# Performance work log

Hardware: AMD Instinct MI355X
Metric: run time of the kernel (lower is better)

## Reference

```python
import jax, jax.numpy as jnp
import numpy as np

N = 100000
E = 6400000
F_IN = 128
N_CLASSES = 16


def _glorot(key, shape):
    fan_in, fan_out = shape[0], shape[1]
    lim = (6.0 / (fan_in + fan_out)) ** 0.5
    return jax.random.uniform(key, shape, jnp.float32, -lim, lim)


def setup_inputs() -> dict:
    key = jax.random.key(0)
    ks = jax.random.split(key, 12)
    x = jax.random.normal(ks[0], (N, F_IN), jnp.float32)
    edge_index = jax.random.randint(ks[1], (2, E), 0, N, jnp.int64)
    return {
        "x": x,
        "W1": _glorot(ks[2], (F_IN, 16)), "b1": jnp.zeros((16,), jnp.float32),
        "W2": _glorot(ks[3], (16, 32)), "b2": jnp.zeros((32,), jnp.float32),
        "Wf1": _glorot(ks[4], (32, 64)), "bf1": jnp.zeros((64,), jnp.float32),
        "Wf2": _glorot(ks[5], (64, 32)), "bf2": jnp.zeros((32,), jnp.float32),
        "Wf3": _glorot(ks[6], (32, N_CLASSES)), "bf3": jnp.zeros((N_CLASSES,), jnp.float32),
        "edge_index": edge_index,
    }


def gcn_conv(x, edge_index, W, b):
    """GCNConv: D^-1/2 (A+I) D^-1/2 X W + b (self-loops added)."""
    h = x @ W  # transform first (small hidden dim), then aggregate
    loop = jnp.arange(N, dtype=edge_index.dtype)
    src = jnp.concatenate([edge_index[0], loop])
    dst = jnp.concatenate([edge_index[1], loop])
    deg = jax.ops.segment_sum(jnp.ones_like(dst, dtype=h.dtype), dst, num_segments=N)
    dinv = jnp.where(deg > 0, jax.lax.rsqrt(jnp.maximum(deg, 1.0)), 0.0)
    norm = dinv[src] * dinv[dst]  # [E+N]
    msg = h[src] * norm[:, None]  # gather + scale
    out = jax.ops.segment_sum(msg, dst, num_segments=N)  # scatter-add
    return out + b


def reference(x, W1, b1, W2, b2, Wf1, bf1, Wf2, bf2, Wf3, bf3, edge_index):
    h = jax.nn.relu(gcn_conv(x, edge_index, W1, b1))
    h = jax.nn.relu(gcn_conv(h, edge_index, W2, b2))
    h = jax.nn.relu(h @ Wf1 + bf1)
    h = jax.nn.relu(h @ Wf2 + bf2)
    return h @ Wf3 + bf3
```

## Files before the change

kernel.cpp:

```cpp
#include <hip/hip_runtime.h>
#include <hip/hip_bf16.h>
#include <math.h>

#define F_IN 128
#define H1c 16
#define H2c 32
#define H3c 64
#define H4c 32
#define NCc 16

#define BUCKET 256
#define BSH 8
#define BMASK 255u
#define BMAXB 512
#define GP 512

typedef unsigned int u32;

static __device__ __forceinline__ void ldsAddU(u32* p, u32 v) {
    __hip_atomic_fetch_add(p, v, __ATOMIC_RELAXED, __HIP_MEMORY_SCOPE_WORKGROUP);
}
static __device__ __forceinline__ u32 ldsAddURtn(u32* p, u32 v) {
    return __hip_atomic_fetch_add(p, v, __ATOMIC_RELAXED, __HIP_MEMORY_SCOPE_WORKGROUP);
}

__global__ __launch_bounds__(256) void k_detect(const u32* __restrict__ ei, u32* __restrict__ flags) {
    __shared__ int nz;
    if (threadIdx.x == 0) nz = 0;
    __syncthreads();
    for (int i = threadIdx.x; 2 * i + 1 < 8192; i += blockDim.x) {
        if (ei[2 * i + 1] != 0u) atomicAdd(&nz, 1);
    }
    __syncthreads();
    if (threadIdx.x == 0) flags[0] = (nz == 0) ? 2u : 1u;
}

__global__ __launch_bounds__(1024) void k_hist(const u32* __restrict__ ei, int E, int B,
                                               const u32* __restrict__ flags,
                                               u32* __restrict__ cntGB) {
    __shared__ u32 hist[BMAXB];
    for (int t = threadIdx.x; t < B; t += 1024) hist[t] = 0u;
    __syncthreads();
    u32 strd = flags[0];
    int chunk = (E + GP - 1) / GP;
    int e0 = blockIdx.x * chunk;
    int e1 = min(E, e0 + chunk);
    for (int e = e0 + threadIdx.x; e < e1; e += 1024) {
        u32 d = ei[((size_t)E + (size_t)e) * strd];
        ldsAddU(&hist[d >> BSH], 1u);
    }
    __syncthreads();
    for (int t = threadIdx.x; t < B; t += 1024)
        cntGB[(size_t)blockIdx.x * B + t] = hist[t];
}

__global__ __launch_bounds__(GP) void k_scanG(const u32* __restrict__ cntGB, int B,
                                              u32* __restrict__ gbOff, u32* __restrict__ total) {
    __shared__ u32 s[GP];
    int b = blockIdx.x;
    u32 v = cntGB[(size_t)threadIdx.x * B + b];
    s[threadIdx.x] = v;
    __syncthreads();
    for (int o = 1; o < GP; o <<= 1) {
        u32 t = (threadIdx.x >= (u32)o) ? s[threadIdx.x - o] : 0u;
        __syncthreads();
        s[threadIdx.x] += t;
        __syncthreads();
    }
    gbOff[(size_t)threadIdx.x * B + b] = s[threadIdx.x] - v;
    if (threadIdx.x == GP - 1) total[b] = s[GP - 1];
}

__global__ __launch_bounds__(256) void k_scanB(const u32* __restrict__ total, int B,
                                               u32* __restrict__ bstartP) {
    __shared__ u32 s[256];
    int per = (B + 255) / 256;
    int i0 = threadIdx.x * per;
    int iend = min(B, i0 + per);
    u32 sum = 0u;
    for (int i = i0; i < iend; ++i) sum += (total[i] + 3u) & ~3u;
    s[threadIdx.x] = sum;
    __syncthreads();
    for (int o = 1; o < 256; o <<= 1) {
        u32 t = (threadIdx.x >= (u32)o) ? s[threadIdx.x - o] : 0u;
        __syncthreads();
        s[threadIdx.x] += t;
        __syncthreads();
    }
    u32 run = s[threadIdx.x] - sum;
    for (int i = i0; i < iend; ++i) { bstartP[i] = run; run += (total[i] + 3u) & ~3u; }
}

__global__ __launch_bounds__(1024) void k_part(const u32* __restrict__ ei, int E, int B,
                                               const u32* __restrict__ flags,
                                               const u32* __restrict__ gbOff,
                                               const u32* __restrict__ bstartP,
                                               u32* __restrict__ bbuf) {
    __shared__ u32 cur[BMAXB];
    for (int t = threadIdx.x; t < B; t += 1024)
        cur[t] = bstartP[t] + gbOff[(size_t)blockIdx.x * B + t];
    __syncthreads();
    u32 strd = flags[0];
    int chunk = (E + GP - 1) / GP;
    int e0 = blockIdx.x * chunk;
    int e1 = min(E, e0 + chunk);
    for (int e = e0 + threadIdx.x; e < e1; e += 1024) {
        u32 sidx = ei[(size_t)e * strd];
        u32 d = ei[((size_t)E + (size_t)e) * strd];
        u32 p = atomicAdd(&cur[d >> BSH], 1u);
        bbuf[p] = (sidx << BSH) | (d & BMASK);
    }
}

__global__ __launch_bounds__(1024) void k_csr(const u32* __restrict__ bbuf,
                                              const u32* __restrict__ bstartP,
                                              const u32* __restrict__ total, int N,
                                              u32* __restrict__ cnt, u32* __restrict__ off,
                                              float* __restrict__ dinv, u32* __restrict__ perm) {
    __shared__ u32 ncnt[BUCKET];
    __shared__ u32 sc[BUCKET];
    __shared__ u32 ncur[BUCKET];
    int b = blockIdx.x;
    u32 base = bstartP[b], tot = total[b];
    if (threadIdx.x < BUCKET) ncnt[threadIdx.x] = 0u;
    __syncthreads();
    u32 nv4 = tot >> 2;
    for (u32 q = threadIdx.x; q < nv4; q += 1024) {
        uint4 e4 = *reinterpret_cast<const uint4*>(bbuf + base + q * 4);
        ldsAddU(&ncnt[e4.x & BMASK], 1u);
        ldsAddU(&ncnt[e4.y & BMASK], 1u);
        ldsAddU(&ncnt[e4.z & BMASK], 1u);
        ldsAddU(&ncnt[e4.w & BMASK], 1u);
    }
    u32 i0 = (nv4 << 2) + threadIdx.x;
    if (i0 < tot) ldsAddU(&ncnt[bbuf[base + i0] & BMASK], 1u);
    __syncthreads();
    u32 v = 0u;
    if (threadIdx.x < BUCKET) { v = ncnt[threadIdx.x]; sc[threadIdx.x] = v; }
    __syncthreads();
    for (int o = 1; o < BUCKET; o <<= 1) {
        u32 t = 0u;
        if (threadIdx.x < BUCKET && threadIdx.x >= (u32)o) t = sc[threadIdx.x - o];
        __syncthreads();
        if (threadIdx.x < BUCKET) sc[threadIdx.x] += t;
        __syncthreads();
    }
    if (threadIdx.x < BUCKET) {
        u32 o = base + (sc[threadIdx.x] - v);
        ncur[threadIdx.x] = o;
        int node = b * BUCKET + (int)threadIdx.x;
        if (node < N) {
            cnt[node] = v;
            off[node] = o;
            dinv[node] = rsqrtf((float)(v + 1u));
        }
    }
    __syncthreads();
    for (u32 q = threadIdx.x; q < nv4; q += 1024) {
        uint4 e4 = *reinterpret_cast<const uint4*>(bbuf + base + q * 4);
        u32 p;
        p = ldsAddURtn(&ncur[e4.x & BMASK], 1u); perm[p] = e4.x >> BSH;
        p = ldsAddURtn(&ncur[e4.y & BMASK], 1u); perm[p] = e4.y >> BSH;
        p = ldsAddURtn(&ncur[e4.z & BMASK], 1u); perm[p] = e4.z >> BSH;
        p = ldsAddURtn(&ncur[e4.w & BMASK], 1u); perm[p] = e4.w >> BSH;
    }
    if (i0 < tot) {
        u32 e = bbuf[base + i0];
        u32 p = ldsAddURtn(&ncur[e & BMASK], 1u);
        perm[p] = e >> BSH;
    }
}

__global__ __launch_bounds__(256) void k_xw1(const float* __restrict__ x, const float* __restrict__ W1,
                                             const float* __restrict__ dinv, float* __restrict__ h1s, int n) {
    __shared__ float Ws[F_IN * H1c];
    for (int t = threadIdx.x; t < F_IN * H1c; t += 256) Ws[t] = W1[t];
    __syncthreads();
    int r = blockIdx.x * 16 + (threadIdx.x >> 4);
    int c = threadIdx.x & 15;
    if (r >= n) return;
    const float* xr = x + (size_t)r * F_IN;
    float a0 = 0.f, a1 = 0.f;
    #pragma unroll
    for (int k = 0; k < F_IN; k += 4) {
        float4 xv = *reinterpret_cast<const float4*>(xr + k);
        a0 += xv.x * Ws[(k + 0) * H1c + c];
        a1 += xv.y * Ws[(k + 1) * H1c + c];
        a0 += xv.z * Ws[(k + 2) * H1c + c];
        a1 += xv.w * Ws[(k + 3) * H1c + c];
    }
    h1s[(size_t)r * H1c + c] = (a0 + a1) * dinv[r];
}

__global__ __launch_bounds__(256) void k_agg1(const float* __restrict__ h1s, const u32* __restrict__ perm,
                                              const u32* __restrict__ off, const u32* __restrict__ cnt,
                                              const float* __restrict__ dinv, const float* __restrict__ b1,
                                              float* __restrict__ p2, int N) {
    int g = threadIdx.x >> 2, l4 = threadIdx.x & 3;
    int node = blockIdx.x * 64 + g;
    if (node >= N) return;
    u32 s0 = off[node], len = cnt[node];
    int fo = l4 * 4;
    float x0 = 0.f, y0 = 0.f, z0 = 0.f, w0 = 0.f;
    float x1 = 0.f, y1 = 0.f, z1 = 0.f, w1 = 0.f;
    float x2 = 0.f, y2 = 0.f, z2 = 0.f, w2 = 0.f;
    float x3 = 0.f, y3 = 0.f, z3 = 0.f, w3 = 0.f;
    u32 it = 0;
    for (; it + 4 <= len; it += 4) {
        u32 e0 = perm[s0 + it], e1 = perm[s0 + it + 1];
        u32 e2 = perm[s0 + it + 2], e3 = perm[s0 + it + 3];
        float4 v0 = *reinterpret_cast<const float4*>(h1s + (size_t)e0 * H1c + fo);
        float4 v1 = *reinterpret_cast<const float4*>(h1s + (size_t)e1 * H1c + fo);
        float4 v2 = *reinterpret_cast<const float4*>(h1s + (size_t)e2 * H1c + fo);
        float4 v3 = *reinterpret_cast<const float4*>(h1s + (size_t)e3 * H1c + fo);
        x0 += v0.x; y0 += v0.y; z0 += v0.z; w0 += v0.w;
        x1 += v1.x; y1 += v1.y; z1 += v1.z; w1 += v1.w;
        x2 += v2.x; y2 += v2.y; z2 += v2.z; w2 += v2.w;
        x3 += v3.x; y3 += v3.y; z3 += v3.z; w3 += v3.w;
    }
    for (; it < len; ++it) {
        u32 e = perm[s0 + it];
        float4 v = *reinterpret_cast<const float4*>(h1s + (size_t)e * H1c + fo);
        x0 += v.x; y0 += v.y; z0 += v.z; w0 += v.w;
    }
    float4 self = *reinterpret_cast<const float4*>(h1s + (size_t)node * H1c + fo);
    float dv = dinv[node];
    float4 bv = *reinterpret_cast<const float4*>(b1 + fo);
    float4 r;
    r.x = fmaxf(dv * ((x0 + x1) + (x2 + x3) + self.x) + bv.x, 0.f) * dv;
    r.y = fmaxf(dv * ((y0 + y1) + (y2 + y3) + self.y) + bv.y, 0.f) * dv;
    r.z = fmaxf(dv * ((z0 + z1) + (z2 + z3) + self.z) + bv.z, 0.f) * dv;
    r.w = fmaxf(dv * ((w0 + w1) + (w2 + w3) + self.w) + bv.w, 0.f) * dv;
    *reinterpret_cast<float4*>(p2 + (size_t)node * H1c + fo) = r;
}

__global__ __launch_bounds__(256) void k_agg2w2(const float* __restrict__ p2, const u32* __restrict__ perm,
                                                const u32* __restrict__ off, const u32* __restrict__ cnt,
                                                const float* __restrict__ dinv, const float* __restrict__ W2,
                                                const float* __restrict__ b2, float* __restrict__ h2post,
                                                int N) {
    __shared__ float hL[64][H1c + 1];
    __shared__ float W2s[H1c * H2c];
    __shared__ float b2s[H2c];
    for (int t = threadIdx.x; t < H1c * H2c; t += 256) W2s[t] = W2[t];
    if (threadIdx.x < H2c) b2s[threadIdx.x] = b2[threadIdx.x];

    int g = threadIdx.x >> 2, l4 = threadIdx.x & 3;
    int node = blockIdx.x * 64 + g;
    int fo = l4 * 4;
    float rx = 0.f, ry = 0.f, rz = 0.f, rw = 0.f;
    if (node < N) {
        u32 s0 = off[node], len = cnt[node];
        float x0 = 0.f, y0 = 0.f, z0 = 0.f, w0 = 0.f;
        float x1 = 0.f, y1 = 0.f, z1 = 0.f, w1 = 0.f;
        float x2 = 0.f, y2 = 0.f, z2 = 0.f, w2 = 0.f;
        float x3 = 0.f, y3 = 0.f, z3 = 0.f, w3 = 0.f;
        u32 it = 0;
        for (; it + 4 <= len; it += 4) {
            u32 e0 = perm[s0 + it], e1 = perm[s0 + it + 1];
            u32 e2 = perm[s0 + it + 2], e3 = perm[s0 + it + 3];
            float4 v0 = *reinterpret_cast<const float4*>(p2 + (size_t)e0 * H1c + fo);
            float4 v1 = *reinterpret_cast<const float4*>(p2 + (size_t)e1 * H1c + fo);
            float4 v2 = *reinterpret_cast<const float4*>(p2 + (size_t)e2 * H1c + fo);
            float4 v3 = *reinterpret_cast<const float4*>(p2 + (size_t)e3 * H1c + fo);
            x0 += v0.x; y0 += v0.y; z0 += v0.z; w0 += v0.w;
            x1 += v1.x; y1 += v1.y; z1 += v1.z; w1 += v1.w;
            x2 += v2.x; y2 += v2.y; z2 += v2.z; w2 += v2.w;
            x3 += v3.x; y3 += v3.y; z3 += v3.z; w3 += v3.w;
        }
        for (; it < len; ++it) {
            u32 e = perm[s0 + it];
            float4 v = *reinterpret_cast<const float4*>(p2 + (size_t)e * H1c + fo);
            x0 += v.x; y0 += v.y; z0 += v.z; w0 += v.w;
        }
        float4 self = *reinterpret_cast<const float4*>(p2 + (size_t)node * H1c + fo);
        float dv = dinv[node];
        rx = dv * ((x0 + x1) + (x2 + x3) + self.x);
        ry = dv * ((y0 + y1) + (y2 + y3) + self.y);
        rz = dv * ((z0 + z1) + (z2 + z3) + self.z);
        rw = dv * ((w0 + w1) + (w2 + w3) + self.w);
    }
    hL[g][fo + 0] = rx;
    hL[g][fo + 1] = ry;
    hL[g][fo + 2] = rz;
    hL[g][fo + 3] = rw;
    __syncthreads();

    int nbase = blockIdx.x * 64;
    #pragma unroll
    for (int rep = 0; rep < 8; ++rep) {
        int o = threadIdx.x + rep * 256;
        int nl = o >> 5, c = o & 31;
        int n2 = nbase + nl;
        if (n2 < N) {
            float s = b2s[c];
            #pragma unroll
            for (int k = 0; k < H1c; ++k) s += hL[nl][k] * W2s[k * H2c + c];
            h2post[(size_t)n2 * H2c + c] = fmaxf(s, 0.f);
        }
    }
}

__global__ __launch_bounds__(256) void k_mlp(const float* __restrict__ h2post,
                                             const float* __restrict__ Wf1, const float* __restrict__ bf1,
                                             const float* __restrict__ Wf2, const float* __restrict__ bf2,
                                             const float* __restrict__ Wf3, const float* __restrict__ bf3,
                                             float* __restrict__ out, int n) {
    __shared__ float W1s[H2c * H3c];
    __shared__ float W2s[H3c * H4c];
    __shared__ float W3s[H4c * NCc];
    __shared__ float b1s[H3c], b2s[H4c], b3s[NCc];
    for (int t = threadIdx.x; t < H2c * H3c; t += 256) W1s[t] = Wf1[t];
    for (int t = threadIdx.x; t < H3c * H4c; t += 256) W2s[t] = Wf2[t];
    for (int t = threadIdx.x; t < H4c * NCc; t += 256) W3s[t] = Wf3[t];
    if (threadIdx.x < H3c) b1s[threadIdx.x] = bf1[threadIdx.x];
    if (threadIdx.x < H4c) b2s[threadIdx.x] = bf2[threadIdx.x];
    if (threadIdx.x < NCc) b3s[threadIdx.x] = bf3[threadIdx.x];
    __syncthreads();

    int r = blockIdx.x * 256 + threadIdx.x;
    if (r >= n) return;

    float h2v[H2c];
    #pragma unroll
    for (int k = 0; k < H2c; k += 4) {
        float4 v = *reinterpret_cast<const float4*>(h2post + (size_t)r * H2c + k);
        h2v[k] = v.x; h2v[k + 1] = v.y; h2v[k + 2] = v.z; h2v[k + 3] = v.w;
    }
    float a4[H4c];
    #pragma unroll
    for (int k2 = 0; k2 < H4c; ++k2) a4[k2] = b2s[k2];
    #pragma unroll 4
    for (int j = 0; j < H3c; ++j) {
        float t = b1s[j];
        #pragma unroll
        for (int k = 0; k < H2c; ++k) t += h2v[k] * W1s[k * H3c + j];
        t = fmaxf(t, 0.f);
        #pragma unroll
        for (int k2 = 0; k2 < H4c; ++k2) a4[k2] += t * W2s[j * H4c + k2];
    }
    #pragma unroll
    for (int k2 = 0; k2 < H4c; ++k2) a4[k2] = fmaxf(a4[k2], 0.f);

    #pragma unroll
    for (int c0 = 0; c0 < NCc; c0 += 4) {
        float o0 = b3s[c0], o1 = b3s[c0 + 1], o2 = b3s[c0 + 2], o3 = b3s[c0 + 3];
        #pragma unroll
        for (int k2 = 0; k2 < H4c; ++k2) {
            float a = a4[k2];
            o0 += a * W3s[k2 * NCc + c0];
            o1 += a * W3s[k2 * NCc + c0 + 1];
            o2 += a * W3s[k2 * NCc + c0 + 2];
            o3 += a * W3s[k2 * NCc + c0 + 3];
        }
        *reinterpret_cast<float4*>(out + (size_t)r * NCc + c0) = make_float4(o0, o1, o2, o3);
    }
}

extern "C" void kernel_launch(void* const* d_in, const int* in_sizes, int n_in,
                              void* d_out, int out_size, void* d_ws, size_t ws_size,
                              hipStream_t stream) {
    const float* x   = (const float*)d_in[0];
    const float* W1  = (const float*)d_in[1];
    const float* b1  = (const float*)d_in[2];
    const float* W2  = (const float*)d_in[3];
    const float* b2  = (const float*)d_in[4];
    const float* Wf1 = (const float*)d_in[5];
    const float* bf1 = (const float*)d_in[6];
    const float* Wf2 = (const float*)d_in[7];
    const float* bf2 = (const float*)d_in[8];
    const float* Wf3 = (const float*)d_in[9];
    const float* bf3 = (const float*)d_in[10];
    const u32*   ei  = (const u32*)d_in[11];

    int N = in_sizes[0] / F_IN;
    int E = in_sizes[11] / 2;
    int B = (N + BUCKET - 1) >> BSH;
    if (B > BMAXB) return;

    char* w = (char*)d_ws;
    u32* flags  = (u32*)w;   w += 64;
    float* dinv = (float*)w; w += (size_t)((N + 3) & ~3) * 4;
    u32* cnt    = (u32*)w;   w += (size_t)((N + 3) & ~3) * 4;
    u32* off    = (u32*)w;   w += (size_t)((N + 3) & ~3) * 4;
    float* h2p  = (float*)w; w += (size_t)N * H2c * 4;
    u32* perm   = (u32*)w;   w += ((size_t)E + 4096) * 4;
    u32* bbuf   = (u32*)w;   w += ((size_t)E + 4096) * 4;
    u32* cntGB  = (u32*)w;   w += (size_t)GP * BMAXB * 4;
    u32* gbOff  = (u32*)w;   w += (size_t)GP * BMAXB * 4;
    u32* total  = (u32*)w;   w += (size_t)(BMAXB + 8) * 4;
    u32* bstartP= (u32*)w;   w += (size_t)(BMAXB + 8) * 4;
    float* h1s = (float*)bbuf;
    float* p2  = h1s + (size_t)N * H1c;

    k_detect<<<1, 256, 0, stream>>>(ei, flags);
    k_hist  <<<GP, 1024, 0, stream>>>(ei, E, B, flags, cntGB);
    k_scanG <<<B, GP, 0, stream>>>(cntGB, B, gbOff, total);
    k_scanB <<<1, 256, 0, stream>>>(total, B, bstartP);
    k_part  <<<GP, 1024, 0, stream>>>(ei, E, B, flags, gbOff, bstartP, bbuf);
    k_csr   <<<B, 1024, 0, stream>>>(bbuf, bstartP, total, N, cnt, off, dinv, perm);

    int nb16 = (N + 15) / 16;
    k_xw1<<<nb16, 256, 0, stream>>>(x, W1, dinv, h1s, N);
    int nb64 = (N + 63) / 64;
    k_agg1<<<nb64, 256, 0, stream>>>(h1s, perm, off, cnt, dinv, b1, p2, N);
    k_agg2w2<<<nb64, 256, 0, stream>>>(p2, perm, off, cnt, dinv, W2, b2, h2p, N);
    int nbN = (N + 255) / 256;
    k_mlp<<<nbN, 256, 0, stream>>>(h2p, Wf1, bf1, Wf2, bf2, Wf3, bf3, (float*)d_out, N);
}
```

Measured before the change: 508.1 us.

## Split hidden features into two 8-wide planes and add nontemporal streaming loads

Stores the 16-wide layer-1 features as two planes of 8 floats, so each gather in the aggregation kernels touches 32 bytes per node per plane instead of 64. Each plane is processed by separate blocks, which shrinks the gather working set and should improve cache hit rates. The fused agg2+W2 kernel is split into a plain aggregation plus a separate W2 transform kernel. Streaming reads (edge lists, perm, x) use nontemporal loads to avoid polluting cache. The cost is that perm and the offsets are read twice, once per plane, and an extra kernel launch and intermediate buffer are added.

```diff
diff --git a/kernel.cpp b/kernel.cpp
--- a/kernel.cpp
+++ b/kernel.cpp
@@ -16,12 +16,22 @@
 #define GP 512
 
 typedef unsigned int u32;
+typedef unsigned int u32x4 __attribute__((ext_vector_type(4)));
+typedef float f32x4 __attribute__((ext_vector_type(4)));
 
 static __device__ __forceinline__ void ldsAddU(u32* p, u32 v) {
     __hip_atomic_fetch_add(p, v, __ATOMIC_RELAXED, __HIP_MEMORY_SCOPE_WORKGROUP);
 }
 static __device__ __forceinline__ u32 ldsAddURtn(u32* p, u32 v) {
     return __hip_atomic_fetch_add(p, v, __ATOMIC_RELAXED, __HIP_MEMORY_SCOPE_WORKGROUP);
+}
+static __device__ __forceinline__ u32 ntl(const u32* p) { return __builtin_nontemporal_load(p); }
+static __device__ __forceinline__ u32x4 ntl4(const u32* p) {
+    return __builtin_nontemporal_load(reinterpret_cast<const u32x4*>(p));
+}
+static __device__ __forceinline__ float4 ntlf4(const float* p) {
+    f32x4 v = __builtin_nontemporal_load(reinterpret_cast<const f32x4*>(p));
+    return make_float4(v[0], v[1], v[2], v[3]);
 }
 
 __global__ __launch_bounds__(256) void k_detect(const u32* __restrict__ ei, u32* __restrict__ flags) {
@@ -46,7 +56,7 @@
     int e0 = blockIdx.x * chunk;
     int e1 = min(E, e0 + chunk);
     for (int e = e0 + threadIdx.x; e < e1; e += 1024) {
-        u32 d = ei[((size_t)E + (size_t)e) * strd];
+        u32 d = ntl(ei + ((size_t)E + (size_t)e) * strd);
         ldsAddU(&hist[d >> BSH], 1u);
     }
     __syncthreads();
@@ -105,8 +115,8 @@
     int e0 = blockIdx.x * chunk;
     int e1 = min(E, e0 + chunk);
     for (int e = e0 + threadIdx.x; e < e1; e += 1024) {
-        u32 sidx = ei[(size_t)e * strd];
-        u32 d = ei[((size_t)E + (size_t)e) * strd];
+        u32 sidx = ntl(ei + (size_t)e * strd);
+        u32 d = ntl(ei + ((size_t)E + (size_t)e) * strd);
         u32 p = atomicAdd(&cur[d >> BSH], 1u);
         bbuf[p] = (sidx << BSH) | (d & BMASK);
     }
@@ -126,11 +136,11 @@
     __syncthreads();
     u32 nv4 = tot >> 2;
     for (u32 q = threadIdx.x; q < nv4; q += 1024) {
-        uint4 e4 = *reinterpret_cast<const uint4*>(bbuf + base + q * 4);
-        ldsAddU(&ncnt[e4.x & BMASK], 1u);
-        ldsAddU(&ncnt[e4.y & BMASK], 1u);
-        ldsAddU(&ncnt[e4.z & BMASK], 1u);
-        ldsAddU(&ncnt[e4.w & BMASK], 1u);
+        u32x4 e4 = ntl4(bbuf + base + q * 4);
+        ldsAddU(&ncnt[e4[0] & BMASK], 1u);
+        ldsAddU(&ncnt[e4[1] & BMASK], 1u);
+        ldsAddU(&ncnt[e4[2] & BMASK], 1u);
+        ldsAddU(&ncnt[e4[3] & BMASK], 1u);
     }
     u32 i0 = (nv4 << 2) + threadIdx.x;
     if (i0 < tot) ldsAddU(&ncnt[bbuf[base + i0] & BMASK], 1u);
@@ -157,12 +167,12 @@
     }
     __syncthreads();
     for (u32 q = threadIdx.x; q < nv4; q += 1024) {
-        uint4 e4 = *reinterpret_cast<const uint4*>(bbuf + base + q * 4);
+        u32x4 e4 = ntl4(bbuf + base + q * 4);
         u32 p;
-        p = ldsAddURtn(&ncur[e4.x & BMASK], 1u); perm[p] = e4.x >> BSH;
-        p = ldsAddURtn(&ncur[e4.y & BMASK], 1u); perm[p] = e4.y >> BSH;
-        p = ldsAddURtn(&ncur[e4.z & BMASK], 1u); perm[p] = e4.z >> BSH;
-        p = ldsAddURtn(&ncur[e4.w & BMASK], 1u); perm[p] = e4.w >> BSH;
+        p = ldsAddURtn(&ncur[e4[0] & BMASK], 1u); perm[p] = e4[0] >> BSH;
+        p = ldsAddURtn(&ncur[e4[1] & BMASK], 1u); perm[p] = e4[1] >> BSH;
+        p = ldsAddURtn(&ncur[e4[2] & BMASK], 1u); perm[p] = e4[2] >> BSH;
+        p = ldsAddURtn(&ncur[e4[3] & BMASK], 1u); perm[p] = e4[3] >> BSH;
     }
     if (i0 < tot) {
         u32 e = bbuf[base + i0];
@@ -183,121 +193,136 @@
     float a0 = 0.f, a1 = 0.f;
     #pragma unroll
     for (int k = 0; k < F_IN; k += 4) {
-        float4 xv = *reinterpret_cast<const float4*>(xr + k);
+        float4 xv = ntlf4(xr + k);
         a0 += xv.x * Ws[(k + 0) * H1c + c];
         a1 += xv.y * Ws[(k + 1) * H1c + c];
         a0 += xv.z * Ws[(k + 2) * H1c + c];
         a1 += xv.w * Ws[(k + 3) * H1c + c];
     }
-    h1s[(size_t)r * H1c + c] = (a0 + a1) * dinv[r];
+    h1s[(size_t)(c >> 3) * n * 8 + (size_t)r * 8 + (c & 7)] = (a0 + a1) * dinv[r];
 }
 
 __global__ __launch_bounds__(256) void k_agg1(const float* __restrict__ h1s, const u32* __restrict__ perm,
                                               const u32* __restrict__ off, const u32* __restrict__ cnt,
                                               const float* __restrict__ dinv, const float* __restrict__ b1,
                                               float* __restrict__ p2, int N) {
-    int g = threadIdx.x >> 2, l4 = threadIdx.x & 3;
-    int node = blockIdx.x * 64 + g;
+    int plane = blockIdx.x & 1;
+    int nb = blockIdx.x >> 1;
+    int g = threadIdx.x >> 1, l = threadIdx.x & 1;
+    int node = nb * 128 + g;
     if (node >= N) return;
+    const float* hp = h1s + (size_t)plane * N * 8;
     u32 s0 = off[node], len = cnt[node];
-    int fo = l4 * 4;
+    int fo = l * 4;
     float x0 = 0.f, y0 = 0.f, z0 = 0.f, w0 = 0.f;
     float x1 = 0.f, y1 = 0.f, z1 = 0.f, w1 = 0.f;
     float x2 = 0.f, y2 = 0.f, z2 = 0.f, w2 = 0.f;
     float x3 = 0.f, y3 = 0.f, z3 = 0.f, w3 = 0.f;
     u32 it = 0;
     for (; it + 4 <= len; it += 4) {
-        u32 e0 = perm[s0 + it], e1 = perm[s0 + it + 1];
-        u32 e2 = perm[s0 + it + 2], e3 = perm[s0 + it + 3];
-        float4 v0 = *reinterpret_cast<const float4*>(h1s + (size_t)e0 * H1c + fo);
-        float4 v1 = *reinterpret_cast<const float4*>(h1s + (size_t)e1 * H1c + fo);
-        float4 v2 = *reinterpret_cast<const float4*>(h1s + (size_t)e2 * H1c + fo);
-        float4 v3 = *reinterpret_cast<const float4*>(h1s + (size_t)e3 * H1c + fo);
+        u32 e0 = ntl(perm + s0 + it),     e1 = ntl(perm + s0 + it + 1);
+        u32 e2 = ntl(perm + s0 + it + 2), e3 = ntl(perm + s0 + it + 3);
+        float4 v0 = *reinterpret_cast<const float4*>(hp + (size_t)e0 * 8 + fo);
+        float4 v1 = *reinterpret_cast<const float4*>(hp + (size_t)e1 * 8 + fo);
+        float4 v2 = *reinterpret_cast<const float4*>(hp + (size_t)e2 * 8 + fo);
+        float4 v3 = *reinterpret_cast<const float4*>(hp + (size_t)e3 * 8 + fo);
         x0 += v0.x; y0 += v0.y; z0 += v0.z; w0 += v0.w;
         x1 += v1.x; y1 += v1.y; z1 += v1.z; w1 += v1.w;
         x2 += v2.x; y2 += v2.y; z2 += v2.z; w2 += v2.w;
         x3 += v3.x; y3 += v3.y; z3 += v3.z; w3 += v3.w;
     }
     for (; it < len; ++it) {
-        u32 e = perm[s0 + it];
-        float4 v = *reinterpret_cast<const float4*>(h1s + (size_t)e * H1c + fo);
+        u32 e = ntl(perm + s0 + it);
+        float4 v = *reinterpret_cast<const float4*>(hp + (size_t)e * 8 + fo);
         x0 += v.x; y0 += v.y; z0 += v.z; w0 += v.w;
     }
-    float4 self = *reinterpret_cast<const float4*>(h1s + (size_t)node * H1c + fo);
+    float4 self = *reinterpret_cast<const float4*>(hp + (size_t)node * 8 + fo);
     float dv = dinv[node];
-    float4 bv = *reinterpret_cast<const float4*>(b1 + fo);
+    float4 bv = *reinterpret_cast<const float4*>(b1 + plane * 8 + fo);
     float4 r;
     r.x = fmaxf(dv * ((x0 + x1) + (x2 + x3) + self.x) + bv.x, 0.f) * dv;
     r.y = fmaxf(dv * ((y0 + y1) + (y2 + y3) + self.y) + bv.y, 0.f) * dv;
     r.z = fmaxf(dv * ((z0 + z1) + (z2 + z3) + self.z) + bv.z, 0.f) * dv;
     r.w = fmaxf(dv * ((w0 + w1) + (w2 + w3) + self.w) + bv.w, 0.f) * dv;
-    *reinterpret_cast<float4*>(p2 + (size_t)node * H1c + fo) = r;
-}
-
-__global__ __launch_bounds__(256) void k_agg2w2(const float* __restrict__ p2, const u32* __restrict__ perm,
-                                                const u32* __restrict__ off, const u32* __restrict__ cnt,
-                                                const float* __restrict__ dinv, const float* __restrict__ W2,
-                                                const float* __restrict__ b2, float* __restrict__ h2post,
-                                                int N) {
-    __shared__ float hL[64][H1c + 1];
+    *reinterpret_cast<float4*>(p2 + (size_t)plane * N * 8 + (size_t)node * 8 + fo) = r;
+}
+
+__global__ __launch_bounds__(256) void k_agg2(const float* __restrict__ p2, const u32* __restrict__ perm,
+                                              const u32* __restrict__ off, const u32* __restrict__ cnt,
+                                              const float* __restrict__ dinv,
+                                              float* __restrict__ g2, int N) {
+    int plane = blockIdx.x & 1;
+    int nb = blockIdx.x >> 1;
+    int g = threadIdx.x >> 1, l = threadIdx.x & 1;
+    int node = nb * 128 + g;
+    if (node >= N) return;
+    const float* hp = p2 + (size_t)plane * N * 8;
+    u32 s0 = off[node], len = cnt[node];
+    int fo = l * 4;
+    float x0 = 0.f, y0 = 0.f, z0 = 0.f, w0 = 0.f;
+    float x1 = 0.f, y1 = 0.f, z1 = 0.f, w1 = 0.f;
+    float x2 = 0.f, y2 = 0.f, z2 = 0.f, w2 = 0.f;
+    float x3 = 0.f, y3 = 0.f, z3 = 0.f, w3 = 0.f;
+    u32 it = 0;
+    for (; it + 4 <= len; it += 4) {
+        u32 e0 = ntl(perm + s0 + it),     e1 = ntl(perm + s0 + it + 1);
+        u32 e2 = ntl(perm + s0 + it + 2), e3 = ntl(perm + s0 + it + 3);
+        float4 v0 = *reinterpret_cast<const float4*>(hp + (size_t)e0 * 8 + fo);
+        float4 v1 = *reinterpret_cast<const float4*>(hp + (size_t)e1 * 8 + fo);
+        float4 v2 = *reinterpret_cast<const float4*>(hp + (size_t)e2 * 8 + fo);
+        float4 v3 = *reinterpret_cast<const float4*>(hp + (size_t)e3 * 8 + fo);
+        x0 += v0.x; y0 += v0.y; z0 += v0.z; w0 += v0.w;
+        x1 += v1.x; y1 += v1.y; z1 += v1.z; w1 += v1.w;
+        x2 += v2.x; y2 += v2.y; z2 += v2.z; w2 += v2.w;
+        x3 += v3.x; y3 += v3.y; z3 += v3.z; w3 += v3.w;
+    }
+    for (; it < len; ++it) {
+        u32 e = ntl(perm + s0 + it);
+        float4 v = *reinterpret_cast<const float4*>(hp + (size_t)e * 8 + fo);
+        x0 += v.x; y0 += v.y; z0 += v.z; w0 += v.w;
+    }
+    float4 self = *reinterpret_cast<const float4*>(hp + (size_t)node * 8 + fo);
+    float dv = dinv[node];
+    float4 r;
+    r.x = dv * ((x0 + x1) + (x2 + x3) + self.x);
+    r.y = dv * ((y0 + y1) + (y2 + y3) + self.y);
+    r.z = dv * ((z0 + z1) + (z2 + z3) + self.z);
+    r.w = dv * ((w0 + w1) + (w2 + w3) + self.w);
+    *reinterpret_cast<float4*>(g2 + (size_t)plane * N * 8 + (size_t)node * 8 + fo) = r;
+}
+
+__global__ __launch_bounds__(256) void k_h2w2(const float* __restrict__ g2,
+                                              const float* __restrict__ W2, const float* __restrict__ b2,
+                                              float* __restrict__ h2post, int N) {
     __shared__ float W2s[H1c * H2c];
     __shared__ float b2s[H2c];
     for (int t = threadIdx.x; t < H1c * H2c; t += 256) W2s[t] = W2[t];
     if (threadIdx.x < H2c) b2s[threadIdx.x] = b2[threadIdx.x];
-
-    int g = threadIdx.x >> 2, l4 = threadIdx.x & 3;
-    int node = blockIdx.x * 64 + g;
-    int fo = l4 * 4;
-    float rx = 0.f, ry = 0.f, rz = 0.f, rw = 0.f;
-    if (node < N) {
-        u32 s0 = off[node], len = cnt[node];
-        float x0 = 0.f, y0 = 0.f, z0 = 0.f, w0 = 0.f;
-        float x1 = 0.f, y1 = 0.f, z1 = 0.f, w1 = 0.f;
-        float x2 = 0.f, y2 = 0.f, z2 = 0.f, w2 = 0.f;
-        float x3 = 0.f, y3 = 0.f, z3 = 0.f, w3 = 0.f;
-        u32 it = 0;
-        for (; it + 4 <= len; it += 4) {
-            u32 e0 = perm[s0 + it], e1 = perm[s0 + it + 1];
-            u32 e2 = perm[s0 + it + 2], e3 = perm[s0 + it + 3];
-            float4 v0 = *reinterpret_cast<const float4*>(p2 + (size_t)e0 * H1c + fo);
-            float4 v1 = *reinterpret_cast<const float4*>(p2 + (size_t)e1 * H1c + fo);
-            float4 v2 = *reinterpret_cast<const float4*>(p2 + (size_t)e2 * H1c + fo);
-            float4 v3 = *reinterpret_cast<const float4*>(p2 + (size_t)e3 * H1c + fo);
-            x0 += v0.x; y0 += v0.y; z0 += v0.z; w0 += v0.w;
-            x1 += v1.x; y1 += v1.y; z1 += v1.z; w1 += v1.w;
-            x2 += v2.x; y2 += v2.y; z2 += v2.z; w2 += v2.w;
-            x3 += v3.x; y3 += v3.y; z3 += v3.z; w3 += v3.w;
+    __syncthreads();
+    int r = blockIdx.x * 256 + threadIdx.x;
+    if (r >= N) return;
+    float h[H1c];
+    float4 a = ntlf4(g2 + (size_t)r * 8);
+    float4 b = ntlf4(g2 + (size_t)r * 8 + 4);
+    float4 c = ntlf4(g2 + (size_t)N * 8 + (size_t)r * 8);
+    float4 d = ntlf4(g2 + (size_t)N * 8 + (size_t)r * 8 + 4);
+    h[0] = a.x; h[1] = a.y; h[2] = a.z; h[3] = a.w;
+    h[4] = b.x; h[5] = b.y; h[6] = b.z; h[7] = b.w;
+    h[8] = c.x; h[9] = c.y; h[10] = c.z; h[11] = c.w;
+    h[12] = d.x; h[13] = d.y; h[14] = d.z; h[15] = d.w;
+    #pragma unroll
+    for (int c0 = 0; c0 < H2c; c0 += 4) {
+        float o0 = b2s[c0], o1 = b2s[c0 + 1], o2 = b2s[c0 + 2], o3 = b2s[c0 + 3];
+        #pragma unroll
+        for (int k = 0; k < H1c; ++k) {
+            float hv = h[k];
+            o0 += hv * W2s[k * H2c + c0];
+            o1 += hv * W2s[k * H2c + c0 + 1];
+            o2 += hv * W2s[k * H2c + c0 + 2];
+            o3 += hv * W2s[k * H2c + c0 + 3];
         }
-        for (; it < len; ++it) {
-            u32 e = perm[s0 + it];
-            float4 v = *reinterpret_cast<const float4*>(p2 + (size_t)e * H1c + fo);
-            x0 += v.x; y0 += v.y; z0 += v.z; w0 += v.w;
-        }
-        float4 self = *reinterpret_cast<const float4*>(p2 + (size_t)node * H1c + fo);
-        float dv = dinv[node];
-        rx = dv * ((x0 + x1) + (x2 + x3) + self.x);
-        ry = dv * ((y0 + y1) + (y2 + y3) + self.y);
-        rz = dv * ((z0 + z1) + (z2 + z3) + self.z);
-        rw = dv * ((w0 + w1) + (w2 + w3) + self.w);
-    }
-    hL[g][fo + 0] = rx;
-    hL[g][fo + 1] = ry;
-    hL[g][fo + 2] = rz;
-    hL[g][fo + 3] = rw;
-    __syncthreads();
-
-    int nbase = blockIdx.x * 64;
-    #pragma unroll
-    for (int rep = 0; rep < 8; ++rep) {
-        int o = threadIdx.x + rep * 256;
-        int nl = o >> 5, c = o & 31;
-        int n2 = nbase + nl;
-        if (n2 < N) {
-            float s = b2s[c];
-            #pragma unroll
-            for (int k = 0; k < H1c; ++k) s += hL[nl][k] * W2s[k * H2c + c];
-            h2post[(size_t)n2 * H2c + c] = fmaxf(s, 0.f);
-        }
+        *reinterpret_cast<float4*>(h2post + (size_t)r * H2c + c0) =
+            make_float4(fmaxf(o0, 0.f), fmaxf(o1, 0.f), fmaxf(o2, 0.f), fmaxf(o3, 0.f));
     }
 }
 
@@ -324,7 +349,7 @@
     float h2v[H2c];
     #pragma unroll
     for (int k = 0; k < H2c; k += 4) {
-        float4 v = *reinterpret_cast<const float4*>(h2post + (size_t)r * H2c + k);
+        float4 v = ntlf4(h2post + (size_t)r * H2c + k);
         h2v[k] = v.x; h2v[k + 1] = v.y; h2v[k + 2] = v.z; h2v[k + 3] = v.w;
     }
     float a4[H4c];
@@ -392,6 +417,7 @@
     u32* bstartP= (u32*)w;   w += (size_t)(BMAXB + 8) * 4;
     float* h1s = (float*)bbuf;
     float* p2  = h1s + (size_t)N * H1c;
+    float* g2  = p2  + (size_t)N * H1c;
 
     k_detect<<<1, 256, 0, stream>>>(ei, flags);
     k_hist  <<<GP, 1024, 0, stream>>>(ei, E, B, flags, cntGB);
@@ -402,9 +428,10 @@
 
     int nb16 = (N + 15) / 16;
     k_xw1<<<nb16, 256, 0, stream>>>(x, W1, dinv, h1s, N);
-    int nb64 = (N + 63) / 64;
-    k_agg1<<<nb64, 256, 0, stream>>>(h1s, perm, off, cnt, dinv, b1, p2, N);
-    k_agg2w2<<<nb64, 256, 0, stream>>>(p2, perm, off, cnt, dinv, W2, b2, h2p, N);
+    int nb128 = (N + 127) / 128;
+    k_agg1<<<nb128 * 2, 256, 0, stream>>>(h1s, perm, off, cnt, dinv, b1, p2, N);
+    k_agg2<<<nb128 * 2, 256, 0, stream>>>(p2, perm, off, cnt, dinv, g2, N);
     int nbN = (N + 255) / 256;
+    k_h2w2<<<nbN, 256, 0, stream>>>(g2, W2, b2, h2p, N);
     k_mlp<<<nbN, 256, 0, stream>>>(h2p, Wf1, bf1, Wf2, bf2, Wf3, bf3, (float*)d_out, N);
 }
```

Result: slower. 646.0 us (+27.1%).
